# Kernel optimization log

Hardware: AMD Instinct MI355X
Metric: run time of the kernel (lower is better)

Reference implementation:

```python
import jax, jax.numpy as jnp
import numpy as np

B, S, HID, NH, HD = 2, 2048, 1024, 16, 64
SCALE = 1.0 / np.sqrt(HD)
NEG = -1e9


def _rope_cache(seq_len, dim, base=10000.0):
    inv_freq = 1.0 / (base ** (np.arange(0, dim, 2, dtype=np.float32) / dim))
    t = np.arange(seq_len, dtype=np.float32)
    freqs = np.outer(t, inv_freq)                      # [S, dim/2]
    emb = np.concatenate([freqs, freqs], axis=-1)      # [S, dim]
    return jnp.asarray(np.cos(emb)), jnp.asarray(np.sin(emb))


def _rotate_half(x):
    x1, x2 = jnp.split(x, 2, axis=-1)
    return jnp.concatenate([-x2, x1], axis=-1)


def setup_inputs() -> dict:
    key = jax.random.key(0)
    k0, k1, k2, k3, k4 = jax.random.split(key, 5)
    hidden_states = jax.random.normal(k0, (B, S, HID), jnp.float32)
    Wq = jax.random.normal(k1, (HID, NH * HD), jnp.float32) * 0.02
    Wk = jax.random.normal(k2, (HID, NH * HD), jnp.float32) * 0.02
    Wv = jax.random.normal(k3, (HID, NH * HD), jnp.float32) * 0.02
    Wo = jax.random.normal(k4, (NH * HD, HID), jnp.float32) * 0.02
    causal = jnp.tril(jnp.ones((S, S), bool))
    attention_mask = jnp.broadcast_to(
        jnp.where(causal, 0.0, NEG).astype(jnp.float32)[None, None], (B, 1, S, S))
    position_ids = jnp.broadcast_to(jnp.arange(S, dtype=jnp.int32)[None], (B, S))
    cos, sin = _rope_cache(S, HD)
    return {"hidden_states": hidden_states, "attention_mask": attention_mask,
            "position_ids": position_ids, "cos": cos, "sin": sin,
            "Wq": Wq, "Wk": Wk, "Wv": Wv, "Wo": Wo}


def reference(hidden_states, attention_mask, position_ids, cos, sin, Wq, Wk, Wv, Wo):
    b, s, _ = hidden_states.shape
    def proj(W):  # [B,S,HID] @ [HID,NH*HD] -> [B,NH,S,HD]
        return jnp.einsum('bsh,hd->bsd', hidden_states, W).reshape(b, s, NH, HD).transpose(0, 2, 1, 3)
    q, k, v = proj(Wq), proj(Wk), proj(Wv)
    # RoPE: gather per-position cos/sin -> [B,1,S,HD]
    cos_g = cos[position_ids][:, None]
    sin_g = sin[position_ids][:, None]
    q = q * cos_g + _rotate_half(q) * sin_g
    k = k * cos_g + _rotate_half(k) * sin_g
    scores = jnp.einsum('bhqd,bhkd->bhqk', q, k) * SCALE + attention_mask
    attn = jax.nn.softmax(scores.astype(jnp.float32), axis=-1).astype(q.dtype)
    out = jnp.einsum('bhqk,bhkd->bhqd', attn, v)
    out = out.transpose(0, 2, 1, 3).reshape(b, s, NH * HD)
    return jnp.einsum('bsd,dh->bsh', out, Wo)
```

## Files before the change

kernel.cpp:

```cpp
#include <hip/hip_runtime.h>

typedef __bf16 bf16x8 __attribute__((ext_vector_type(8)));
typedef float  f32x4  __attribute__((ext_vector_type(4)));
typedef unsigned short ushortx8 __attribute__((ext_vector_type(8)));
typedef unsigned short ushortx4 __attribute__((ext_vector_type(4)));

static __device__ __forceinline__ unsigned short f2bf(float f) {
  unsigned int u = __builtin_bit_cast(unsigned int, f);
  u += 0x7FFFu + ((u >> 16) & 1u);
  return (unsigned short)(u >> 16);
}
static __device__ __forceinline__ unsigned short f2bf_fast(float f) {
  unsigned int u = __builtin_bit_cast(unsigned int, f);
  return (unsigned short)((u + 0x8000u) >> 16);
}

#define GLL16(gp, lp) __builtin_amdgcn_global_load_lds(                       \
    (const __attribute__((address_space(1))) void*)(gp),                      \
    (__attribute__((address_space(3))) void*)(lp), 16, 0, 0)

__global__ __launch_bounds__(256) void prep_kernel(const float* __restrict__ X,
                                                   const float* __restrict__ W0,
                                                   const float* __restrict__ W1,
                                                   const float* __restrict__ W2,
                                                   const float* __restrict__ W3,
                                                   unsigned short* __restrict__ Xbf,
                                                   unsigned short* __restrict__ D0,
                                                   unsigned short* __restrict__ D1,
                                                   unsigned short* __restrict__ D2,
                                                   unsigned short* __restrict__ D3) {
  int z = blockIdx.z;
  if (z >= 4) {
    long bid = (long)(z - 4) * 1024 + blockIdx.y * 32 + blockIdx.x;
    int tl = threadIdx.y * 32 + threadIdx.x;
    long i = bid * 2048 + (long)tl * 8;
    float4 f0 = *(const float4*)(X + i);
    float4 f1 = *(const float4*)(X + i + 4);
    ushortx8 u;
    u[0] = f2bf(f0.x); u[1] = f2bf(f0.y); u[2] = f2bf(f0.z); u[3] = f2bf(f0.w);
    u[4] = f2bf(f1.x); u[5] = f2bf(f1.y); u[6] = f2bf(f1.z); u[7] = f2bf(f1.w);
    *(ushortx8*)(Xbf + i) = u;
    return;
  }
  const float* src = (z == 0) ? W0 : (z == 1) ? W1 : (z == 2) ? W2 : W3;
  unsigned short* dst = (z == 0) ? D0 : (z == 1) ? D1 : (z == 2) ? D2 : D3;
  const int R = 1024, C = 1024;
  __shared__ unsigned short t[32][33];
  int c = blockIdx.x * 32 + threadIdx.x;
#pragma unroll
  for (int i = 0; i < 4; ++i) {
    int r = blockIdx.y * 32 + threadIdx.y + i * 8;
    t[threadIdx.y + i * 8][threadIdx.x] = f2bf(src[(size_t)r * C + c]);
  }
  __syncthreads();
  int rr = blockIdx.y * 32 + threadIdx.x;
#pragma unroll
  for (int i = 0; i < 4; ++i) {
    int cc = blockIdx.x * 32 + threadIdx.y + i * 8;
    dst[(size_t)cc * R + rr] = t[threadIdx.x][threadIdx.y + i * 8];
  }
}

__global__ __launch_bounds__(256) void tpose_kernel(const unsigned short* __restrict__ src,
                                                    unsigned short* __restrict__ dst,
                                                    int R, int C) {
  size_t moff = (size_t)blockIdx.z * (size_t)R * (size_t)C;
  src += moff; dst += moff;
  __shared__ unsigned short t[32][33];
  int c = blockIdx.x * 32 + threadIdx.x;
#pragma unroll
  for (int i = 0; i < 4; ++i) {
    int r = blockIdx.y * 32 + threadIdx.y + i * 8;
    t[threadIdx.y + i * 8][threadIdx.x] = src[(size_t)r * C + c];
  }
  __syncthreads();
  int rr = blockIdx.y * 32 + threadIdx.x;
#pragma unroll
  for (int i = 0; i < 4; ++i) {
    int cc = blockIdx.x * 32 + threadIdx.y + i * 8;
    dst[(size_t)cc * R + rr] = t[threadIdx.x][threadIdx.y + i * 8];
  }
}

template <int MODE>
__global__ __launch_bounds__(256) void gemm128_kernel(
    const unsigned short* __restrict__ A,
    const unsigned short* __restrict__ BT0,
    const unsigned short* __restrict__ BT1,
    const unsigned short* __restrict__ BT2,
    float* __restrict__ outF,
    unsigned short* __restrict__ outQ,
    unsigned short* __restrict__ outK,
    unsigned short* __restrict__ outV,
    const int* __restrict__ pos_ids,
    const float* __restrict__ cosb,
    const float* __restrict__ sinb) {
  const int K = 1024, N = 1024;
  int z = blockIdx.z;
  const unsigned short* BT = (MODE == 0 || z == 0) ? BT0 : (z == 1 ? BT1 : BT2);
  int n0 = blockIdx.x * 128, m0 = blockIdx.y * 128;
  int t = threadIdx.x, lane = t & 63, w = t >> 6;
  int wy = w >> 1, wx = w & 1;
  int n16 = lane & 15, quad = lane >> 4;
  __shared__ __align__(16) unsigned short sA0[128 * 64];
  __shared__ __align__(16) unsigned short sA1[128 * 64];
  __shared__ __align__(16) unsigned short sB0[128 * 64];
  __shared__ __align__(16) unsigned short sB1[128 * 64];

  int r8 = lane >> 3, c8 = lane & 7;
  int srow = w * 32 + r8;
  const char* gA = (const char*)(A + (size_t)(m0 + srow) * K) + (c8 ^ r8) * 16;
  const char* gB = (const char*)(BT + (size_t)(n0 + srow) * K) + (c8 ^ r8) * 16;

  f32x4 acc[4][4];
#pragma unroll
  for (int i = 0; i < 4; ++i)
#pragma unroll
    for (int j = 0; j < 4; ++j) acc[i][j] = f32x4{0.f, 0.f, 0.f, 0.f};

#define GSTAGE(kk_, SA, SB)                                                     \
  do {                                                                          \
    _Pragma("unroll") for (int i = 0; i < 4; ++i) {                             \
      GLL16(gA + (size_t)(kk_) * 2 + (size_t)i * 8 * K * 2,                     \
            SA + (w * 32 + i * 8) * 64);                                        \
      GLL16(gB + (size_t)(kk_) * 2 + (size_t)i * 8 * K * 2,                     \
            SB + (w * 32 + i * 8) * 64);                                        \
    }                                                                           \
  } while (0)

#define GCOMPUTE(SA, SB)                                                        \
  do {                                                                          \
    _Pragma("unroll") for (int kb = 0; kb < 2; ++kb) {                          \
      bf16x8 a[4], b[4];                                                        \
      _Pragma("unroll") for (int i = 0; i < 4; ++i) {                           \
        int ra = wy * 64 + i * 16 + n16;                                        \
        int rb = wx * 64 + i * 16 + n16;                                        \
        int cs = ((kb * 4 + quad) ^ (n16 & 7)) * 8;                             \
        a[i] = *(const bf16x8*)(&SA[ra * 64 + cs]);                             \
        b[i] = *(const bf16x8*)(&SB[rb * 64 + cs]);                             \
      }                                                                         \
      _Pragma("unroll") for (int mt = 0; mt < 4; ++mt)                          \
        _Pragma("unroll") for (int nt = 0; nt < 4; ++nt)                        \
          acc[mt][nt] =                                                         \
              __builtin_amdgcn_mfma_f32_16x16x32_bf16(a[mt], b[nt],             \
                                                      acc[mt][nt], 0, 0, 0);    \
    }                                                                           \
  } while (0)

  GSTAGE(0, sA0, sB0);
  for (int kk = 0; kk < K;) {
    __syncthreads();
    if (kk + 64 < K) GSTAGE(kk + 64, sA1, sB1);
    GCOMPUTE(sA0, sB0);
    kk += 64;
    if (kk >= K) break;
    __syncthreads();
    if (kk + 64 < K) GSTAGE(kk + 64, sA0, sB0);
    GCOMPUTE(sA1, sB1);
    kk += 64;
  }
#undef GSTAGE
#undef GCOMPUTE

  if (MODE == 1 && z < 2) {
#pragma unroll
    for (int mt = 0; mt < 4; ++mt)
#pragma unroll
      for (int r = 0; r < 4; ++r) {
        int row = m0 + wy * 64 + mt * 16 + quad * 4 + r;
        int b = row >> 11, s = row & 2047;
        int pos = pos_ids[b * 2048 + s];
        const float* cb = cosb + (size_t)pos * 64;
        const float* sb = sinb + (size_t)pos * 64;
#pragma unroll
        for (int nt = 0; nt < 2; ++nt) {
          int d0 = nt * 16 + n16;
          float c0 = cb[d0], s0 = sb[d0], c1 = cb[d0 + 32], s1 = sb[d0 + 32];
          float x0 = acc[mt][nt][r], x1 = acc[mt][nt + 2][r];
          acc[mt][nt][r]     = x0 * c0 - x1 * s0;
          acc[mt][nt + 2][r] = x1 * c1 + x0 * s1;
        }
      }
  }

#pragma unroll
  for (int mt = 0; mt < 4; ++mt)
#pragma unroll
    for (int nt = 0; nt < 4; ++nt)
#pragma unroll
      for (int r = 0; r < 4; ++r) {
        int row = m0 + wy * 64 + mt * 16 + quad * 4 + r;
        int col = n0 + wx * 64 + nt * 16 + n16;
        float v = acc[mt][nt][r];
        if (MODE == 0) {
          outF[(size_t)row * N + col] = v;
        } else {
          unsigned short* dst = (z == 0) ? outQ : (z == 1 ? outK : outV);
          int b = row >> 11, s = row & 2047, h = col >> 6, d = col & 63;
          dst[(((size_t)b * 16 + h) * 2048 + s) * 64 + d] = f2bf(v);
        }
      }
}

__global__ __launch_bounds__(512) void attn_kernel(const unsigned short* __restrict__ Q,
                                                   const unsigned short* __restrict__ Kk,
                                                   const unsigned short* __restrict__ VT,
                                                   unsigned short* __restrict__ O) {
  int bh = blockIdx.x;
  int qt = (int)(gridDim.y - 1 - blockIdx.y);
  int t = threadIdx.x;
  int lane = t & 63;
  int w = t >> 6;
  int g = w >> 2;
  int w4 = w & 3;
  int n16 = lane & 15, quad = lane >> 4;
  int r8 = lane >> 3, c8 = lane & 7;
  const unsigned short* Qb = Q + (size_t)bh * 2048 * 64;
  const unsigned short* Kb = Kk + (size_t)bh * 2048 * 64;
  const unsigned short* Vb = VT + (size_t)bh * 64 * 2048;

  __shared__ __align__(16) unsigned short sKV[2 * 2 * 2 * 4096];
  __shared__ __align__(16) unsigned short sP[8][16 * 64];
  unsigned short* spW = sP[w];
  unsigned short* gBase = sKV + g * 16384;

  const float SCL2 = 0.125f * 1.44269504088896340736f;
  int b_ = bh >> 4, h_ = bh & 15;
  int nk = qt + 1;
  int u = (nk + 1) >> 1;
  int beg = g ? u : 0;
  int end = g ? nk : u;
  int qg = qt * 64 + w4 * 16 + n16;

  bf16x8 aQ[2];
#pragma unroll
  for (int kb = 0; kb < 2; ++kb)
    aQ[kb] = *(const bf16x8*)(Qb + (size_t)qg * 64 + kb * 32 + quad * 8);

  f32x4 o[4];
  float mst = -3e38f, lst = 0.f;
#pragma unroll
  for (int ct = 0; ct < 4; ++ct) o[ct] = f32x4{0.f, 0.f, 0.f, 0.f};

#define ASTAGE(kt_, BUF)                                                                  \
  do {                                                                                    \
    const unsigned short* kg_ = Kb + (size_t)((kt_) * 64 + w4 * 16) * 64;                 \
    const unsigned short* vg_ = Vb + (size_t)(w4 * 16) * 2048 + (kt_) * 64;               \
    unsigned short* dK = gBase + (BUF) * 8192 + (w4 * 16) * 64;                           \
    unsigned short* dV = dK + 4096;                                                       \
    GLL16(kg_ + (size_t)r8 * 64 + (c8 ^ r8) * 8, dK);                                     \
    GLL16(kg_ + (size_t)(8 + r8) * 64 + (c8 ^ r8) * 8, dK + 8 * 64);                      \
    GLL16(vg_ + (size_t)r8 * 2048 + (c8 ^ r8) * 8, dV);                                   \
    GLL16(vg_ + (size_t)(8 + r8) * 2048 + (c8 ^ r8) * 8, dV + 8 * 64);                    \
  } while (0)

#define ACOMPUTE(kt_, BUF)                                                                \
  do {                                                                                    \
    const unsigned short* kB_ = gBase + (BUF) * 8192 + (w4 * 16) * 64 - (w4 * 16) * 64;   \
    const unsigned short* kT_ = gBase + (BUF) * 8192;                                     \
    const unsigned short* vT_ = kT_ + 4096;                                               \
    (void)kB_;                                                                            \
    f32x4 sc[4];                                \
    _Pragma("unroll") for (int mt = 0; mt < 4; ++mt) {                                    \
      const unsigned short* kr = &kT_[(mt * 16 + n16) * 64];                              \
      bf16x8 ka0 = *(const bf16x8*)(kr + ((quad ^ (n16 & 7)) * 8));                       \
      bf16x8 ka1 = *(const bf16x8*)(kr + (((4 + quad) ^ (n16 & 7)) * 8));                 \
      f32x4 zv = f32x4{0.f, 0.f, 0.f, 0.f};                                               \
      zv = __builtin_amdgcn_mfma_f32_16x16x32_bf16(ka0, aQ[0], zv, 0, 0, 0);              \
      sc[mt] = __builtin_amdgcn_mfma_f32_16x16x32_bf16(ka1, aQ[1], zv, 0, 0, 0);          \
    }                                                                                     \
    float p[4][4];                                                                        \
    _Pragma("unroll") for (int mt = 0; mt < 4; ++mt)                                      \
      _Pragma("unroll") for (int r = 0; r < 4; ++r) p[mt][r] = sc[mt][r] * SCL2;          \
    if ((kt_) == nk - 1) {                                 \
      int kb0 = (kt_) * 64 + quad * 4;                                                    \
      _Pragma("unroll") for (int mt = 0; mt < 4; ++mt)                                    \
        _Pragma("unroll") for (int r = 0; r < 4; ++r)                                     \
          if (kb0 + mt * 16 + r > qg) p[mt][r] = -3e38f;                                  \
    }                                                                                     \
    float rm = p[0][0];                                                                   \
    _Pragma("unroll") for (int mt = 0; mt < 4; ++mt)                                      \
      _Pragma("unroll") for (int r = 0; r < 4; ++r) rm = fmaxf(rm, p[mt][r]);             \
    rm = fmaxf(rm, __shfl_xor(rm, 16));                                                   \
    rm = fmaxf(rm, __shfl_xor(rm, 32));                                                   \
    float mn = fmaxf(mst, rm);                                                            \
    float al = exp2f(mst - mn);                                                           \
    mst = mn;                                                                             \
    float rs = 0.f;                                                                       \
    _Pragma("unroll") for (int mt = 0; mt < 4; ++mt)                                      \
      _Pragma("unroll") for (int r = 0; r < 4; ++r) {                                     \
        p[mt][r] = exp2f(p[mt][r] - mn);                                                  \
        rs += p[mt][r];                                                                   \
      }                                                                                   \
    lst = lst * al + rs;                                                                  \
    _Pragma("unroll") for (int ct = 0; ct < 4; ++ct)                                      \
      _Pragma("unroll") for (int r = 0; r < 4; ++r) o[ct][r] *= al;                       \
    _Pragma("unroll") for (int mt = 0; mt < 4; ++mt) {                                    \
      ushortx4 uu;                                                                        \
      _Pragma("unroll") for (int r = 0; r < 4; ++r) uu[r] = f2bf_fast(p[mt][r]);          \
      int ch = (mt * 2 + (quad >> 1)) ^ (n16 & 7);                                        \
      *(ushortx4*)(&spW[n16 * 64 + ch * 8 + (quad & 1) * 4]) = uu;                        \
    }                                                                                     \
    __builtin_amdgcn_s_waitcnt(0xC07F);     \
    bf16x8 aP0 = *(const bf16x8*)(&spW[n16 * 64 + ((quad ^ (n16 & 7)) * 8)]);             \
    bf16x8 aP1 = *(const bf16x8*)(&spW[n16 * 64 + (((4 + quad) ^ (n16 & 7)) * 8)]);       \
    _Pragma("unroll") for (int ct = 0; ct < 4; ++ct) {                                    \
      const unsigned short* vr = &vT_[(ct * 16 + n16) * 64];                              \
      bf16x8 va0 = *(const bf16x8*)(vr + ((quad ^ (n16 & 7)) * 8));                       \
      bf16x8 va1 = *(const bf16x8*)(vr + (((4 + quad) ^ (n16 & 7)) * 8));                 \
      o[ct] = __builtin_amdgcn_mfma_f32_16x16x32_bf16(va0, aP0, o[ct], 0, 0, 0);          \
      o[ct] = __builtin_amdgcn_mfma_f32_16x16x32_bf16(va1, aP1, o[ct], 0, 0, 0);          \
    }                                                                                     \
  } while (0)

  if (beg < end) ASTAGE(beg, 0);
  int it = 0;
  while (it < u) {
    __syncthreads();
    {
      int kt = beg + it;
      if (kt + 1 < end) ASTAGE(kt + 1, 1);
      if (kt < end) ACOMPUTE(kt, 0);
    }
    if (++it >= u) break;
    __syncthreads();
    {
      int kt = beg + it;
      if (kt + 1 < end) ASTAGE(kt + 1, 0);
      if (kt < end) ACOMPUTE(kt, 1);
    }
    ++it;
  }
#undef ASTAGE
#undef ACOMPUTE

  lst += __shfl_xor(lst, 16);
  lst += __shfl_xor(lst, 32);

  __syncthreads();
  float* scratch = (float*)sKV;
  int sidx = (w4 * 64 + lane) * 18;
  if (g == 1) {
#pragma unroll
    for (int ct = 0; ct < 4; ++ct)
#pragma unroll
      for (int r = 0; r < 4; ++r) scratch[sidx + ct * 4 + r] = o[ct][r];
    scratch[sidx + 16] = mst;
    scratch[sidx + 17] = lst;
  }
  __syncthreads();
  if (g == 0) {
    float m1 = scratch[sidx + 16], l1 = scratch[sidx + 17];
    float m = fmaxf(mst, m1);
    float a0 = exp2f(mst - m), a1 = exp2f(m1 - m);
    float inv = 1.0f / (lst * a0 + l1 * a1);
#pragma unroll
    for (int ct = 0; ct < 4; ++ct) {
      ushortx4 uo;
#pragma unroll
      for (int r = 0; r < 4; ++r) {
        float v = (o[ct][r] * a0 + scratch[sidx + ct * 4 + r] * a1) * inv;
        uo[r] = f2bf(v);
      }
      size_t addr = ((size_t)b_ * 2048 + qg) * 1024 + h_ * 64 + ct * 16 + quad * 4;
      *(ushortx4*)(&O[addr]) = uo;
    }
  }
}

extern "C" void kernel_launch(void* const* d_in, const int* in_sizes, int n_in,
                              void* d_out, int out_size, void* d_ws, size_t ws_size,
                              hipStream_t stream) {
  const float* X    = (const float*)d_in[0];
  const int*   pos  = (const int*)d_in[2];
  const float* cosb = (const float*)d_in[3];
  const float* sinb = (const float*)d_in[4];
  const float* Wq   = (const float*)d_in[5];
  const float* Wk   = (const float*)d_in[6];
  const float* Wv   = (const float*)d_in[7];
  const float* Wo   = (const float*)d_in[8];
  float* out = (float*)d_out;

  char* ws = (char*)d_ws;
  const size_t SZ_X = 4096UL * 1024 * 2;
  const size_t SZ_W = 1024UL * 1024 * 2;
  unsigned short* Xbf = (unsigned short*)(ws);
  unsigned short* WTq = (unsigned short*)(ws + SZ_X);
  unsigned short* WTk = (unsigned short*)(ws + SZ_X + SZ_W);
  unsigned short* WTv = (unsigned short*)(ws + SZ_X + 2 * SZ_W);
  unsigned short* WTo = (unsigned short*)(ws + SZ_X + 3 * SZ_W);
  unsigned short* Qbf = (unsigned short*)(ws + SZ_X + 4 * SZ_W);
  unsigned short* Kbf = (unsigned short*)(ws + 2 * SZ_X + 4 * SZ_W);
  unsigned short* Vbf = (unsigned short*)(ws + 3 * SZ_X + 4 * SZ_W);
  unsigned short* VTr = (unsigned short*)(ws + 4 * SZ_X + 4 * SZ_W);
  unsigned short* Obf = (unsigned short*)(ws + 5 * SZ_X + 4 * SZ_W);

  prep_kernel<<<dim3(32, 32, 6), dim3(32, 8), 0, stream>>>(
      X, Wq, Wk, Wv, Wo, Xbf, WTq, WTk, WTv, WTo);

  gemm128_kernel<1><<<dim3(8, 32, 3), 256, 0, stream>>>(Xbf, WTq, WTk, WTv,
                                                        nullptr, Qbf, Kbf, Vbf,
                                                        pos, cosb, sinb);

  tpose_kernel<<<dim3(2, 64, 32), dim3(32, 8), 0, stream>>>(Vbf, VTr, 2048, 64);

  attn_kernel<<<dim3(32, 32), 512, 0, stream>>>(Qbf, Kbf, VTr, Obf);

  gemm128_kernel<0><<<dim3(8, 32, 1), 256, 0, stream>>>(Obf, WTo, nullptr, nullptr,
                                                        out, nullptr, nullptr, nullptr,
                                                        nullptr, nullptr, nullptr);
}
```

Before: 230.0 us.

## Fuse V transpose into QKV GEMM epilogue and simplify GEMM pipeline

The QKV projection GEMM now writes V directly in transposed [B,H,D,S] layout, so the separate transpose kernel and its extra buffer round trip are removed. Block indices are remapped so the M tile varies fastest, changing which blocks run together and how B tiles are reused. The GEMM main loop goes from double-buffered LDS staging to a single buffer with two barriers per step. That halves LDS use but drops the overlap of global loads with MFMA compute.

```diff
diff --git a/kernel.cpp b/kernel.cpp
--- a/kernel.cpp
+++ b/kernel.cpp
@@ -61,27 +61,6 @@
   }
 }
 
-__global__ __launch_bounds__(256) void tpose_kernel(const unsigned short* __restrict__ src,
-                                                    unsigned short* __restrict__ dst,
-                                                    int R, int C) {
-  size_t moff = (size_t)blockIdx.z * (size_t)R * (size_t)C;
-  src += moff; dst += moff;
-  __shared__ unsigned short t[32][33];
-  int c = blockIdx.x * 32 + threadIdx.x;
-#pragma unroll
-  for (int i = 0; i < 4; ++i) {
-    int r = blockIdx.y * 32 + threadIdx.y + i * 8;
-    t[threadIdx.y + i * 8][threadIdx.x] = src[(size_t)r * C + c];
-  }
-  __syncthreads();
-  int rr = blockIdx.y * 32 + threadIdx.x;
-#pragma unroll
-  for (int i = 0; i < 4; ++i) {
-    int cc = blockIdx.x * 32 + threadIdx.y + i * 8;
-    dst[(size_t)cc * R + rr] = t[threadIdx.x][threadIdx.y + i * 8];
-  }
-}
-
 template <int MODE>
 __global__ __launch_bounds__(256) void gemm128_kernel(
     const unsigned short* __restrict__ A,
@@ -91,21 +70,23 @@
     float* __restrict__ outF,
     unsigned short* __restrict__ outQ,
     unsigned short* __restrict__ outK,
-    unsigned short* __restrict__ outV,
+    unsigned short* __restrict__ outVT,
     const int* __restrict__ pos_ids,
     const float* __restrict__ cosb,
     const float* __restrict__ sinb) {
   const int K = 1024, N = 1024;
-  int z = blockIdx.z;
+  int id = blockIdx.x + 8 * (blockIdx.y + 32 * blockIdx.z);
+  int m_idx = id & 31;
+  int nzi = id >> 5;
+  int n_idx = (MODE == 1) ? (nzi & 7) : nzi;
+  int z = (MODE == 1) ? (nzi >> 3) : 0;
   const unsigned short* BT = (MODE == 0 || z == 0) ? BT0 : (z == 1 ? BT1 : BT2);
-  int n0 = blockIdx.x * 128, m0 = blockIdx.y * 128;
+  int n0 = n_idx * 128, m0 = m_idx * 128;
   int t = threadIdx.x, lane = t & 63, w = t >> 6;
   int wy = w >> 1, wx = w & 1;
   int n16 = lane & 15, quad = lane >> 4;
-  __shared__ __align__(16) unsigned short sA0[128 * 64];
-  __shared__ __align__(16) unsigned short sA1[128 * 64];
-  __shared__ __align__(16) unsigned short sB0[128 * 64];
-  __shared__ __align__(16) unsigned short sB1[128 * 64];
+  __shared__ __align__(16) unsigned short sA[128 * 64];
+  __shared__ __align__(16) unsigned short sB[128 * 64];
 
   int r8 = lane >> 3, c8 = lane & 7;
   int srow = w * 32 + r8;
@@ -118,49 +99,32 @@
 #pragma unroll
     for (int j = 0; j < 4; ++j) acc[i][j] = f32x4{0.f, 0.f, 0.f, 0.f};
 
-#define GSTAGE(kk_, SA, SB)                                                     \
-  do {                                                                          \
-    _Pragma("unroll") for (int i = 0; i < 4; ++i) {                             \
-      GLL16(gA + (size_t)(kk_) * 2 + (size_t)i * 8 * K * 2,                     \
-            SA + (w * 32 + i * 8) * 64);                                        \
-      GLL16(gB + (size_t)(kk_) * 2 + (size_t)i * 8 * K * 2,                     \
-            SB + (w * 32 + i * 8) * 64);                                        \
-    }                                                                           \
-  } while (0)
-
-#define GCOMPUTE(SA, SB)                                                        \
-  do {                                                                          \
-    _Pragma("unroll") for (int kb = 0; kb < 2; ++kb) {                          \
-      bf16x8 a[4], b[4];                                                        \
-      _Pragma("unroll") for (int i = 0; i < 4; ++i) {                           \
-        int ra = wy * 64 + i * 16 + n16;                                        \
-        int rb = wx * 64 + i * 16 + n16;                                        \
-        int cs = ((kb * 4 + quad) ^ (n16 & 7)) * 8;                             \
-        a[i] = *(const bf16x8*)(&SA[ra * 64 + cs]);                             \
-        b[i] = *(const bf16x8*)(&SB[rb * 64 + cs]);                             \
-      }                                                                         \
-      _Pragma("unroll") for (int mt = 0; mt < 4; ++mt)                          \
-        _Pragma("unroll") for (int nt = 0; nt < 4; ++nt)                        \
-          acc[mt][nt] =                                                         \
-              __builtin_amdgcn_mfma_f32_16x16x32_bf16(a[mt], b[nt],             \
-                                                      acc[mt][nt], 0, 0, 0);    \
-    }                                                                           \
-  } while (0)
-
-  GSTAGE(0, sA0, sB0);
-  for (int kk = 0; kk < K;) {
+  for (int kk = 0; kk < K; kk += 64) {
     __syncthreads();
-    if (kk + 64 < K) GSTAGE(kk + 64, sA1, sB1);
-    GCOMPUTE(sA0, sB0);
-    kk += 64;
-    if (kk >= K) break;
+#pragma unroll
+    for (int i = 0; i < 4; ++i) {
+      GLL16(gA + (size_t)kk * 2 + (size_t)i * 8 * K * 2, sA + (w * 32 + i * 8) * 64);
+      GLL16(gB + (size_t)kk * 2 + (size_t)i * 8 * K * 2, sB + (w * 32 + i * 8) * 64);
+    }
     __syncthreads();
-    if (kk + 64 < K) GSTAGE(kk + 64, sA0, sB0);
-    GCOMPUTE(sA1, sB1);
-    kk += 64;
-  }
-#undef GSTAGE
-#undef GCOMPUTE
+#pragma unroll
+    for (int kb = 0; kb < 2; ++kb) {
+      bf16x8 a[4], b[4];
+#pragma unroll
+      for (int i = 0; i < 4; ++i) {
+        int ra = wy * 64 + i * 16 + n16;
+        int rb = wx * 64 + i * 16 + n16;
+        int cs = ((kb * 4 + quad) ^ (n16 & 7)) * 8;
+        a[i] = *(const bf16x8*)(&sA[ra * 64 + cs]);
+        b[i] = *(const bf16x8*)(&sB[rb * 64 + cs]);
+      }
+#pragma unroll
+      for (int mt = 0; mt < 4; ++mt)
+#pragma unroll
+        for (int nt = 0; nt < 4; ++nt)
+          acc[mt][nt] = __builtin_amdgcn_mfma_f32_16x16x32_bf16(a[mt], b[nt], acc[mt][nt], 0, 0, 0);
+    }
+  }
 
   if (MODE == 1 && z < 2) {
 #pragma unroll
@@ -183,6 +147,23 @@
       }
   }
 
+  if (MODE == 1 && z == 2) {
+#pragma unroll
+    for (int mt = 0; mt < 4; ++mt)
+#pragma unroll
+      for (int nt = 0; nt < 4; ++nt) {
+        int row = m0 + wy * 64 + mt * 16 + quad * 4;
+        int b = row >> 11, s = row & 2047;
+        int col = n0 + wx * 64 + nt * 16 + n16;
+        int h = col >> 6, d = col & 63;
+        ushortx4 u;
+#pragma unroll
+        for (int r = 0; r < 4; ++r) u[r] = f2bf(acc[mt][nt][r]);
+        *(ushortx4*)(&outVT[(((size_t)b * 16 + h) * 64 + d) * 2048 + s]) = u;
+      }
+    return;
+  }
+
 #pragma unroll
   for (int mt = 0; mt < 4; ++mt)
 #pragma unroll
@@ -195,7 +176,7 @@
         if (MODE == 0) {
           outF[(size_t)row * N + col] = v;
         } else {
-          unsigned short* dst = (z == 0) ? outQ : (z == 1 ? outK : outV);
+          unsigned short* dst = (z == 0) ? outQ : outK;
           int b = row >> 11, s = row & 2047, h = col >> 6, d = col & 63;
           dst[(((size_t)b * 16 + h) * 2048 + s) * 64 + d] = f2bf(v);
         }
@@ -256,10 +237,8 @@
 
 #define ACOMPUTE(kt_, BUF)                                                                \
   do {                                                                                    \
-    const unsigned short* kB_ = gBase + (BUF) * 8192 + (w4 * 16) * 64 - (w4 * 16) * 64;   \
     const unsigned short* kT_ = gBase + (BUF) * 8192;                                     \
     const unsigned short* vT_ = kT_ + 4096;                                               \
-    (void)kB_;                                                                            \
     f32x4 sc[4];                                \
     _Pragma("unroll") for (int mt = 0; mt < 4; ++mt) {                                    \
       const unsigned short* kr = &kT_[(mt * 16 + n16) * 64];                              \
@@ -391,18 +370,15 @@
   unsigned short* WTo = (unsigned short*)(ws + SZ_X + 3 * SZ_W);
   unsigned short* Qbf = (unsigned short*)(ws + SZ_X + 4 * SZ_W);
   unsigned short* Kbf = (unsigned short*)(ws + 2 * SZ_X + 4 * SZ_W);
-  unsigned short* Vbf = (unsigned short*)(ws + 3 * SZ_X + 4 * SZ_W);
-  unsigned short* VTr = (unsigned short*)(ws + 4 * SZ_X + 4 * SZ_W);
-  unsigned short* Obf = (unsigned short*)(ws + 5 * SZ_X + 4 * SZ_W);
+  unsigned short* VTr = (unsigned short*)(ws + 3 * SZ_X + 4 * SZ_W);
+  unsigned short* Obf = (unsigned short*)(ws + 4 * SZ_X + 4 * SZ_W);
 
   prep_kernel<<<dim3(32, 32, 6), dim3(32, 8), 0, stream>>>(
       X, Wq, Wk, Wv, Wo, Xbf, WTq, WTk, WTv, WTo);
 
   gemm128_kernel<1><<<dim3(8, 32, 3), 256, 0, stream>>>(Xbf, WTq, WTk, WTv,
-                                                        nullptr, Qbf, Kbf, Vbf,
+                                                        nullptr, Qbf, Kbf, VTr,
                                                         pos, cosb, sinb);
-
-  tpose_kernel<<<dim3(2, 64, 32), dim3(32, 8), 0, stream>>>(Vbf, VTr, 2048, 64);
 
   attn_kernel<<<dim3(32, 32), 512, 0, stream>>>(Qbf, Kbf, VTr, Obf);
 
```

Measured after the change: 220.1 us. 4.3% less time.
